# Kernel tuning notes

Measured on AMD Instinct MI355X. Metric: run time of the kernel, lower is better.

The kernel has to match this reference:

```python
import jax, jax.numpy as jnp
import numpy as np

HEADS = 16

def setup_inputs() -> dict:
    key = jax.random.key(0)
    ks = jax.random.split(key, 7)
    B, S, E = 2, 2048, 1024
    return {
        "query": jax.random.normal(ks[0], (B, S, E), dtype=jnp.float32),
        "key": jax.random.normal(ks[1], (B, S, E), dtype=jnp.float32),
        "value": jax.random.normal(ks[2], (B, S, E), dtype=jnp.float32),
        "Wqkv": jax.random.normal(ks[3], (E, 3 * E), dtype=jnp.float32) * (E ** -0.5),
        "bqkv": jax.random.normal(ks[4], (3 * E,), dtype=jnp.float32) * 0.02,
        "Wproj": jax.random.normal(ks[5], (E, E), dtype=jnp.float32) * (E ** -0.5),
        "bproj": jax.random.normal(ks[6], (E,), dtype=jnp.float32) * 0.02,
    }

def reference(query, key, value, Wqkv, bqkv, Wproj, bproj):
    # key/value args are unused in the original forward (overwritten by QKV split)
    B, S, E = query.shape
    H = HEADS
    hd = E // H
    qkv = query @ Wqkv + bqkv                     # [B, S, 3E]
    qkv = qkv.reshape(B, S, H, 3 * hd).transpose(0, 2, 1, 3)  # [B, H, S, 3hd]
    q = qkv[..., :hd]
    k = qkv[..., hd:2 * hd]
    v = qkv[..., 2 * hd:]
    qk = jnp.einsum("bhqd,bhkd->bhqk", q, k)
    # faithful quirk: original divides by head_dim**-0.5, i.e. multiplies by sqrt(hd)
    scaled = qk / (hd ** -0.5)
    attn = jax.nn.softmax(scaled, axis=-1)        # dropout p=0 -> identity
    out = jnp.einsum("bhqk,bhkd->bhqd", attn, v)  # [B, H, S, hd]
    out = out.transpose(0, 2, 1, 3).reshape(B, S, E)
    return out @ Wproj + bproj
```

## Files before the change

### kernel.cpp

```cpp
#include <hip/hip_runtime.h>
#include <hip/hip_bf16.h>
#include <stdint.h>

typedef __attribute__((ext_vector_type(8))) _Float16 f16x8;
typedef __attribute__((ext_vector_type(4))) _Float16 f16x4;
typedef __attribute__((ext_vector_type(4))) float f32x4;

static constexpr int BATCH = 2;
static constexpr int SEQ = 2048;
static constexpr int EMB = 1024;
static constexpr int NH = 16;
static constexpr int HD_ = 64;

#define AS1 __attribute__((address_space(1)))
#define AS3 __attribute__((address_space(3)))

__device__ __forceinline__ void gload_lds16(const void* g, void* l) {
  __builtin_amdgcn_global_load_lds((const AS1 uint32_t*)g, (AS3 uint32_t*)l, 16, 0, 0);
}

__device__ __forceinline__ f32x4 mfma16(f16x8 a, f16x8 b, f32x4 c) {
  return __builtin_amdgcn_mfma_f32_16x16x32_f16(a, b, c, 0, 0, 0);
}

__device__ __forceinline__ f16x8 swzread(const _Float16* base, int row, int blk) {
  return *(const f16x8*)((const char*)base + row * 128 +
                         ((blk * 16) ^ ((row & 7) << 4)));
}

__global__ __launch_bounds__(256) void k_convert(const float* __restrict__ in,
                                                 _Float16* __restrict__ oh, int n4) {
  int idx = blockIdx.x * 256 + threadIdx.x;
  if (idx >= n4) return;
  float4 v = reinterpret_cast<const float4*>(in)[idx];
  const float* f = reinterpret_cast<const float*>(&v);
  _Float16 h[4];
#pragma unroll
  for (int i = 0; i < 4; ++i) h[i] = (_Float16)f[i];
  reinterpret_cast<uint2*>(oh)[idx] = *reinterpret_cast<uint2*>(h);
}

template <int PERM>
__global__ __launch_bounds__(256) void k_transpose(const float* __restrict__ in,
                                                   _Float16* __restrict__ out, int R,
                                                   int C) {
  __shared__ float tile[32][33];
  const int t = threadIdx.x;
  const int tr = t >> 5, tc = t & 31;
  const int r0 = blockIdx.y * 32, c0 = blockIdx.x * 32;
#pragma unroll
  for (int rr = 0; rr < 32; rr += 8)
    tile[tr + rr][tc] = in[(size_t)(r0 + tr + rr) * C + c0 + tc];
  __syncthreads();
#pragma unroll
  for (int rr = 0; rr < 32; rr += 8) {
    const int c = c0 + tr + rr;
    int d = c;
    if constexpr (PERM) {
      const int h = c / 192, r = c - h * 192;
      d = (r < 64) ? h * 64 + r
                   : (r < 128 ? 1024 + h * 64 + (r - 64) : 2048 + h * 64 + (r - 128));
    }
    out[(size_t)d * R + r0 + tc] = (_Float16)tile[tc][tr + rr];
  }
}

__global__ __launch_bounds__(256) void k_gemm_qkv(const _Float16* __restrict__ A,
                                                  const _Float16* __restrict__ Bt,
                                                  const float* __restrict__ bias,
                                                  _Float16* __restrict__ oq,
                                                  _Float16* __restrict__ ok,
                                                  _Float16* __restrict__ ov) {
  constexpr int K = EMB;
  __shared__ _Float16 As[2][128 * 32];
  __shared__ _Float16 Bs[2][128 * 32];
  const int t = threadIdx.x;
  const int l = t & 63, w = t >> 6;
  const int lr = l & 15, lg = l >> 4;
  const int wr = w >> 1, wc = w & 1;
  const int m0 = blockIdx.y * 128, n0 = blockIdx.x * 128;

  auto stage = [&](int buf, int k0) {
#pragma unroll
    for (int j = 0; j < 2; ++j) {
      const int c = t + 256 * j;
      const int row = c >> 2, cb = c & 3;
      gload_lds16(A + (size_t)(m0 + row) * K + k0 + cb * 8, &As[buf][c * 8]);
      gload_lds16(Bt + (size_t)(n0 + row) * K + k0 + cb * 8, &Bs[buf][c * 8]);
    }
  };

  f32x4 acc[4][4];
#pragma unroll
  for (int m = 0; m < 4; ++m)
#pragma unroll
    for (int n = 0; n < 4; ++n) acc[m][n] = f32x4{0.f, 0.f, 0.f, 0.f};

  stage(0, 0);
  const int NT = K / 32;
  int cur = 0;
  for (int kt = 0; kt < NT; ++kt) {
    __syncthreads();
    if (kt + 1 < NT) stage(cur ^ 1, (kt + 1) * 32);
    f16x8 af[4], bf[4];
#pragma unroll
    for (int m = 0; m < 4; ++m)
      af[m] = *(const f16x8*)&As[cur][(wr * 64 + m * 16 + lr) * 32 + lg * 8];
#pragma unroll
    for (int n = 0; n < 4; ++n)
      bf[n] = *(const f16x8*)&Bs[cur][(wc * 64 + n * 16 + lr) * 32 + lg * 8];
#pragma unroll
    for (int m = 0; m < 4; ++m)
#pragma unroll
      for (int n = 0; n < 4; ++n) acc[m][n] = mfma16(af[m], bf[n], acc[m][n]);
    cur ^= 1;
  }

  const int sec = n0 >> 10;
#pragma unroll
  for (int m = 0; m < 4; ++m) {
#pragma unroll
    for (int n = 0; n < 4; ++n) {
      const int col = n0 + wc * 64 + n * 16 + lr;
      const int cc = col & 1023;
      const int h = cc >> 6, r = cc & 63;
      const float bv = bias[h * 192 + sec * 64 + r];
      const int row0 = m0 + wr * 64 + m * 16 + lg * 4;
      const int b = row0 >> 11, s0 = row0 & (SEQ - 1);
      if (sec == 2) {
        f16x4 vv;
#pragma unroll
        for (int i = 0; i < 4; ++i) vv[i] = (_Float16)(acc[m][n][i] + bv);
        *(f16x4*)&ov[(((size_t)b * NH + h) * HD_ + r) * SEQ + s0] = vv;
      } else {
#pragma unroll
        for (int i = 0; i < 4; ++i) {
          const float v = acc[m][n][i] + bv;
          const size_t dst = (((size_t)b * NH + h) * SEQ + s0 + i) * HD_ + r;
          if (sec == 0)
            oq[dst] = (_Float16)(v * 11.5415603f);
          else
            ok[dst] = (_Float16)v;
        }
      }
    }
  }
}

__global__ __launch_bounds__(256) void k_gemm_proj(const _Float16* __restrict__ A,
                                                   const _Float16* __restrict__ Bt,
                                                   const float* __restrict__ bias,
                                                   float* __restrict__ of) {
  constexpr int K = EMB, N = EMB;
  __shared__ _Float16 As[2][128 * 32];
  __shared__ _Float16 Bs[2][128 * 32];
  const int t = threadIdx.x;
  const int l = t & 63, w = t >> 6;
  const int lr = l & 15, lg = l >> 4;
  const int wr = w >> 1, wc = w & 1;
  const int m0 = blockIdx.y * 128, n0 = blockIdx.x * 128;

  auto stage = [&](int buf, int k0) {
#pragma unroll
    for (int j = 0; j < 2; ++j) {
      const int c = t + 256 * j;
      const int row = c >> 2, cb = c & 3;
      gload_lds16(A + (size_t)(m0 + row) * K + k0 + cb * 8, &As[buf][c * 8]);
      gload_lds16(Bt + (size_t)(n0 + row) * K + k0 + cb * 8, &Bs[buf][c * 8]);
    }
  };

  f32x4 acc[4][4];
#pragma unroll
  for (int m = 0; m < 4; ++m)
#pragma unroll
    for (int n = 0; n < 4; ++n) acc[m][n] = f32x4{0.f, 0.f, 0.f, 0.f};

  stage(0, 0);
  const int NT = K / 32;
  int cur = 0;
  for (int kt = 0; kt < NT; ++kt) {
    __syncthreads();
    if (kt + 1 < NT) stage(cur ^ 1, (kt + 1) * 32);
    f16x8 af[4], bf[4];
#pragma unroll
    for (int m = 0; m < 4; ++m)
      af[m] = *(const f16x8*)&As[cur][(wr * 64 + m * 16 + lr) * 32 + lg * 8];
#pragma unroll
    for (int n = 0; n < 4; ++n)
      bf[n] = *(const f16x8*)&Bs[cur][(wc * 64 + n * 16 + lr) * 32 + lg * 8];
#pragma unroll
    for (int m = 0; m < 4; ++m)
#pragma unroll
      for (int n = 0; n < 4; ++n) acc[m][n] = mfma16(af[m], bf[n], acc[m][n]);
    cur ^= 1;
  }

#pragma unroll
  for (int m = 0; m < 4; ++m)
#pragma unroll
    for (int n = 0; n < 4; ++n)
#pragma unroll
      for (int i = 0; i < 4; ++i) {
        const int row = m0 + wr * 64 + m * 16 + lg * 4 + i;
        const int col = n0 + wc * 64 + n * 16 + lr;
        of[(size_t)row * N + col] = acc[m][n][i] + bias[col];
      }
}

__global__ __launch_bounds__(512) void k_attn(
    const _Float16* __restrict__ qs, const _Float16* __restrict__ ks,
    const _Float16* __restrict__ vt, _Float16* __restrict__ op,
    float* __restrict__ marr, float* __restrict__ larr) {
  __shared__ _Float16 Kt[2][64][64];
  __shared__ _Float16 Vt[2][64][64];
  __shared__ _Float16 Pl[8][16][64];
  const int t = threadIdx.x;
  const int l = t & 63, w = t >> 6;
  const int lr = l & 15, lg = l >> 4;
  const int id = blockIdx.x;
  const int xc = id & 7, m_ = id >> 3;
  const int kvh = m_ & 1;
  const int bh = xc + 8 * (m_ >> 5);
  const int qb = ((m_ >> 1) & 15) * 128 + w * 16;
  const int kvbase = kvh * (SEQ / 2);

  const size_t qoff = ((size_t)bh * SEQ + qb + lr) * HD_;
  const f16x8 qf0 = *(const f16x8*)(qs + qoff + lg * 8);
  const f16x8 qf1 = *(const f16x8*)(qs + qoff + 32 + lg * 8);

  const _Float16* kbase = ks + (size_t)bh * SEQ * HD_;
  const _Float16* vbase = vt + (size_t)bh * HD_ * SEQ;

  const int srow = t >> 3, scb = t & 7;
  auto stage = [&](const int buf, const int kv0) {
    gload_lds16(kbase + (size_t)(kv0 + srow) * HD_ + (scb ^ (srow & 7)) * 8,
                &Kt[buf][srow][scb * 8]);
    gload_lds16(vbase + (size_t)srow * SEQ + kv0 + (scb ^ (srow & 7)) * 8,
                &Vt[buf][srow][scb * 8]);
  };

  stage(0, kvbase);

  float mr = -1e30f, lsum = 0.f;
  f32x4 oacc[4];
#pragma unroll
  for (int n = 0; n < 4; ++n) oacc[n] = f32x4{0.f, 0.f, 0.f, 0.f};

  const int NT = SEQ / 128;
  for (int it = 0; it < NT; ++it) {
    const int cur = it & 1;
    __syncthreads();
    if (it + 1 < NT) stage(cur ^ 1, kvbase + (it + 1) * 64);

    f32x4 sa[4];
    __builtin_amdgcn_s_setprio(1);
#pragma unroll
    for (int t4 = 0; t4 < 4; ++t4) {
      const int r = t4 * 16 + lr;
      const f16x8 kf0 = swzread(&Kt[cur][0][0], r, lg);
      const f16x8 kf1 = swzread(&Kt[cur][0][0], r, lg + 4);
      f32x4 s = mfma16(kf0, qf0, f32x4{0.f, 0.f, 0.f, 0.f});
      sa[t4] = mfma16(kf1, qf1, s);
    }
    __builtin_amdgcn_s_setprio(0);

    float t01 = fmaxf(fmaxf(sa[0][0], sa[0][1]), fmaxf(sa[0][2], sa[0][3]));
    float t23 = fmaxf(fmaxf(sa[1][0], sa[1][1]), fmaxf(sa[1][2], sa[1][3]));
    float t45 = fmaxf(fmaxf(sa[2][0], sa[2][1]), fmaxf(sa[2][2], sa[2][3]));
    float t67 = fmaxf(fmaxf(sa[3][0], sa[3][1]), fmaxf(sa[3][2], sa[3][3]));
    float tm = fmaxf(fmaxf(t01, t23), fmaxf(t45, t67));
    tm = fmaxf(tm, __shfl_xor(tm, 16));
    tm = fmaxf(tm, __shfl_xor(tm, 32));

    if (__all(tm < mr - 24.0f)) continue;

    if (__any(tm > mr + 8.0f)) {
      const float nm = fmaxf(mr, tm);
      const float corr = exp2f(mr - nm);
      mr = nm;
      lsum *= corr;
      float cb4[4];
#pragma unroll
      for (int i = 0; i < 4; ++i)
        cb4[i] = __shfl(corr, (l & 48) + ((l >> 4) << 2) + i);
#pragma unroll
      for (int n = 0; n < 4; ++n)
#pragma unroll
        for (int i = 0; i < 4; ++i) oacc[n][i] *= cb4[i];
    }

    float ts = 0.f;
    char* plbase = (char*)&Pl[w][0][0];
#pragma unroll
    for (int t4 = 0; t4 < 4; ++t4) {
      f16x4 pp;
#pragma unroll
      for (int i = 0; i < 4; ++i) {
        const float p = exp2f(sa[t4][i] - mr);
        ts += p;
        pp[i] = (_Float16)p;
      }
      *(f16x4*)(plbase + lr * 128 + ((t4 * 32 + lg * 8) ^ ((lr & 7) << 4))) = pp;
    }
    ts += __shfl_xor(ts, 16);
    ts += __shfl_xor(ts, 32);
    lsum += ts;

    const f16x8 aP0 = swzread(&Pl[w][0][0], lr, lg);
    const f16x8 aP1 = swzread(&Pl[w][0][0], lr, lg + 4);
    __builtin_amdgcn_s_setprio(1);
#pragma unroll
    for (int n = 0; n < 4; ++n) {
      const int d = n * 16 + lr;
      const f16x8 bv0 = swzread(&Vt[cur][0][0], d, lg);
      const f16x8 bv1 = swzread(&Vt[cur][0][0], d, lg + 4);
      oacc[n] = mfma16(aP0, bv0, oacc[n]);
      oacc[n] = mfma16(aP1, bv1, oacc[n]);
    }
    __builtin_amdgcn_s_setprio(0);
  }

  const size_t mlbase = ((size_t)kvh * 32 + bh) * SEQ + qb;
  if (l < 16) {
    marr[mlbase + l] = mr;
    larr[mlbase + l] = lsum;
  }
  _Float16* opb = op + (size_t)kvh * BATCH * SEQ * EMB;
  const int b = bh >> 4, h = bh & 15;
#pragma unroll
  for (int n = 0; n < 4; ++n)
#pragma unroll
    for (int i = 0; i < 4; ++i) {
      const int row = qb + ((l >> 4) << 2) + i;
      opb[((size_t)b * SEQ + row) * EMB + h * HD_ + n * 16 + lr] =
          (_Float16)oacc[n][i];
    }
}

__global__ __launch_bounds__(256) void k_combine(const _Float16* __restrict__ op,
                                                 const float* __restrict__ marr,
                                                 const float* __restrict__ larr,
                                                 _Float16* __restrict__ ao) {
  const int idx = blockIdx.x * 256 + threadIdx.x;
  const int e8 = idx & 127;
  const size_t rs = (size_t)(idx >> 7);
  const int h = e8 >> 3;
  const int b = (int)(rs >> 11);
  const size_t s = rs & (SEQ - 1);
  const size_t mi = ((size_t)b * NH + h) * SEQ + s;
  const float m1 = marr[mi], l1 = larr[mi];
  const float m2 = marr[(size_t)32 * SEQ + mi], l2 = larr[(size_t)32 * SEQ + mi];
  const float mx = fmaxf(m1, m2);
  const float w1 = exp2f(m1 - mx), w2 = exp2f(m2 - mx);
  const float inv = 1.0f / (l1 * w1 + l2 * w2);
  const f16x8 o1 = ((const f16x8*)op)[idx];
  const f16x8 o2 = ((const f16x8*)op)[idx + (BATCH * SEQ * EMB / 8)];
  f16x8 r;
#pragma unroll
  for (int j = 0; j < 8; ++j)
    r[j] = (_Float16)(((float)o1[j] * w1 + (float)o2[j] * w2) * inv);
  ((f16x8*)ao)[idx] = r;
}

extern "C" void kernel_launch(void* const* d_in, const int* in_sizes, int n_in,
                              void* d_out, int out_size, void* d_ws, size_t ws_size,
                              hipStream_t stream) {
  const float* query = (const float*)d_in[0];
  const float* Wqkv = (const float*)d_in[3];
  const float* bqkv = (const float*)d_in[4];
  const float* Wproj = (const float*)d_in[5];
  const float* bproj = (const float*)d_in[6];
  float* out = (float*)d_out;

  char* ws = (char*)d_ws;
  const size_t MB = 1024 * 1024;
  _Float16* q_f16   = (_Float16*)(ws + 0);
  _Float16* Wqkv_t  = (_Float16*)(ws + 16 * MB);
  _Float16* q_s     = (_Float16*)(ws + 24 * MB);
  _Float16* k_s     = (_Float16*)(ws + 32 * MB);
  _Float16* v_t     = (_Float16*)(ws + 40 * MB);
  _Float16* op      = (_Float16*)(ws + 0);
  _Float16* Wproj_t = (_Float16*)(ws + 48 * MB);
  float*    marr    = (float*)(ws + 50 * MB);
  float*    larr    = (float*)(ws + 50 * MB + 512 * 1024);
  _Float16* a_o     = (_Float16*)(ws + 51 * MB);

  const int M = BATCH * SEQ;
  k_convert<<<(M * EMB / 4 + 255) / 256, 256, 0, stream>>>(query, q_f16, M * EMB / 4);
  k_transpose<1><<<dim3(3 * EMB / 32, EMB / 32), 256, 0, stream>>>(Wqkv, Wqkv_t, EMB,
                                                                   3 * EMB);
  k_gemm_qkv<<<dim3(24, M / 128), 256, 0, stream>>>(q_f16, Wqkv_t, bqkv, q_s, k_s, v_t);
  k_transpose<0><<<dim3(EMB / 32, EMB / 32), 256, 0, stream>>>(Wproj, Wproj_t, EMB, EMB);
  k_attn<<<dim3(1024), 512, 0, stream>>>(q_s, k_s, v_t, op, marr, larr);
  k_combine<<<dim3(BATCH * SEQ * EMB / 8 / 256), 256, 0, stream>>>(op, marr, larr, a_o);
  k_gemm_proj<<<dim3(EMB / 128, M / 128), 256, 0, stream>>>(a_o, Wproj_t, bproj, out);
}
```

Baseline: 156.4 us.

## Fuse prep kernels into one launch and split P·V into two halves

Merges the fp16 conversion of the query and both weight transposes into one kernel indexed by block id, which removes two kernel launches and their gaps. In the attention kernel, the P tile is now written and consumed in two 32-column halves through a smaller per-warp LDS buffer with a new swizzle, interleaving the exp computation with the P·V MFMAs. This cuts shared memory use and may allow overlap between the exp work and the matrix ops. The cost is a branchy prep kernel with a runtime perm flag and extra LDS round trips per iteration.

```diff
diff --git a/kernel.cpp b/kernel.cpp
--- a/kernel.cpp
+++ b/kernel.cpp
@@ -28,26 +28,42 @@
                          ((blk * 16) ^ ((row & 7) << 4)));
 }
 
-__global__ __launch_bounds__(256) void k_convert(const float* __restrict__ in,
-                                                 _Float16* __restrict__ oh, int n4) {
-  int idx = blockIdx.x * 256 + threadIdx.x;
-  if (idx >= n4) return;
-  float4 v = reinterpret_cast<const float4*>(in)[idx];
-  const float* f = reinterpret_cast<const float*>(&v);
-  _Float16 h[4];
-#pragma unroll
-  for (int i = 0; i < 4; ++i) h[i] = (_Float16)f[i];
-  reinterpret_cast<uint2*>(oh)[idx] = *reinterpret_cast<uint2*>(h);
-}
-
-template <int PERM>
-__global__ __launch_bounds__(256) void k_transpose(const float* __restrict__ in,
-                                                   _Float16* __restrict__ out, int R,
-                                                   int C) {
+__global__ __launch_bounds__(256) void k_prep(const float* __restrict__ q,
+                                              _Float16* __restrict__ qo,
+                                              const float* __restrict__ wqkv,
+                                              _Float16* __restrict__ wqkvo,
+                                              const float* __restrict__ wproj,
+                                              _Float16* __restrict__ wprojo) {
   __shared__ float tile[32][33];
+  const int blk = blockIdx.x;
   const int t = threadIdx.x;
+  if (blk < 4096) {
+    const int idx = blk * 256 + t;
+    float4 v = reinterpret_cast<const float4*>(q)[idx];
+    const float* f = reinterpret_cast<const float*>(&v);
+    _Float16 h[4];
+#pragma unroll
+    for (int i = 0; i < 4; ++i) h[i] = (_Float16)f[i];
+    reinterpret_cast<uint2*>(qo)[idx] = *reinterpret_cast<uint2*>(h);
+    return;
+  }
+  const float* in;
+  _Float16* out;
+  int R, C, bx, by;
+  bool perm;
+  if (blk < 4096 + 3072) {
+    const int lo = blk - 4096;
+    bx = lo % 96;
+    by = lo / 96;
+    in = wqkv; out = wqkvo; R = 1024; C = 3072; perm = true;
+  } else {
+    const int lo = blk - 7168;
+    bx = lo & 31;
+    by = lo >> 5;
+    in = wproj; out = wprojo; R = 1024; C = 1024; perm = false;
+  }
   const int tr = t >> 5, tc = t & 31;
-  const int r0 = blockIdx.y * 32, c0 = blockIdx.x * 32;
+  const int r0 = by * 32, c0 = bx * 32;
 #pragma unroll
   for (int rr = 0; rr < 32; rr += 8)
     tile[tr + rr][tc] = in[(size_t)(r0 + tr + rr) * C + c0 + tc];
@@ -56,7 +72,7 @@
   for (int rr = 0; rr < 32; rr += 8) {
     const int c = c0 + tr + rr;
     int d = c;
-    if constexpr (PERM) {
+    if (perm) {
       const int h = c / 192, r = c - h * 192;
       d = (r < 64) ? h * 64 + r
                    : (r < 128 ? 1024 + h * 64 + (r - 64) : 2048 + h * 64 + (r - 128));
@@ -214,7 +230,7 @@
     float* __restrict__ marr, float* __restrict__ larr) {
   __shared__ _Float16 Kt[2][64][64];
   __shared__ _Float16 Vt[2][64][64];
-  __shared__ _Float16 Pl[8][16][64];
+  __shared__ _Float16 Plh[8][16][32];
   const int t = threadIdx.x;
   const int l = t & 63, w = t >> 6;
   const int lr = l & 15, lg = l >> 4;
@@ -247,6 +263,9 @@
 #pragma unroll
   for (int n = 0; n < 4; ++n) oacc[n] = f32x4{0.f, 0.f, 0.f, 0.f};
 
+  char* plbase = (char*)&Plh[w][0][0];
+  const int plswz = ((lr >> 1) & 3) << 4;
+
   const int NT = SEQ / 128;
   for (int it = 0; it < NT; ++it) {
     const int cur = it & 1;
@@ -291,34 +310,33 @@
     }
 
     float ts = 0.f;
-    char* plbase = (char*)&Pl[w][0][0];
-#pragma unroll
-    for (int t4 = 0; t4 < 4; ++t4) {
-      f16x4 pp;
-#pragma unroll
-      for (int i = 0; i < 4; ++i) {
-        const float p = exp2f(sa[t4][i] - mr);
-        ts += p;
-        pp[i] = (_Float16)p;
+#pragma unroll
+    for (int H = 0; H < 2; ++H) {
+#pragma unroll
+      for (int th = 0; th < 2; ++th) {
+        const int t4 = 2 * H + th;
+        f16x4 pp;
+#pragma unroll
+        for (int i = 0; i < 4; ++i) {
+          const float p = exp2f(sa[t4][i] - mr);
+          ts += p;
+          pp[i] = (_Float16)p;
+        }
+        *(f16x4*)(plbase + lr * 64 + ((th * 32 + lg * 8) ^ plswz)) = pp;
       }
-      *(f16x4*)(plbase + lr * 128 + ((t4 * 32 + lg * 8) ^ ((lr & 7) << 4))) = pp;
+      const f16x8 aP = *(const f16x8*)(plbase + lr * 64 + ((lg * 16) ^ plswz));
+      __builtin_amdgcn_s_setprio(1);
+#pragma unroll
+      for (int n = 0; n < 4; ++n) {
+        const int d = n * 16 + lr;
+        const f16x8 bv = swzread(&Vt[cur][0][0], d, lg + 4 * H);
+        oacc[n] = mfma16(aP, bv, oacc[n]);
+      }
+      __builtin_amdgcn_s_setprio(0);
     }
     ts += __shfl_xor(ts, 16);
     ts += __shfl_xor(ts, 32);
     lsum += ts;
-
-    const f16x8 aP0 = swzread(&Pl[w][0][0], lr, lg);
-    const f16x8 aP1 = swzread(&Pl[w][0][0], lr, lg + 4);
-    __builtin_amdgcn_s_setprio(1);
-#pragma unroll
-    for (int n = 0; n < 4; ++n) {
-      const int d = n * 16 + lr;
-      const f16x8 bv0 = swzread(&Vt[cur][0][0], d, lg);
-      const f16x8 bv1 = swzread(&Vt[cur][0][0], d, lg + 4);
-      oacc[n] = mfma16(aP0, bv0, oacc[n]);
-      oacc[n] = mfma16(aP1, bv1, oacc[n]);
-    }
-    __builtin_amdgcn_s_setprio(0);
   }
 
   const size_t mlbase = ((size_t)kvh * 32 + bh) * SEQ + qb;
@@ -387,11 +405,8 @@
   _Float16* a_o     = (_Float16*)(ws + 51 * MB);
 
   const int M = BATCH * SEQ;
-  k_convert<<<(M * EMB / 4 + 255) / 256, 256, 0, stream>>>(query, q_f16, M * EMB / 4);
-  k_transpose<1><<<dim3(3 * EMB / 32, EMB / 32), 256, 0, stream>>>(Wqkv, Wqkv_t, EMB,
-                                                                   3 * EMB);
+  k_prep<<<dim3(8192), 256, 0, stream>>>(query, q_f16, Wqkv, Wqkv_t, Wproj, Wproj_t);
   k_gemm_qkv<<<dim3(24, M / 128), 256, 0, stream>>>(q_f16, Wqkv_t, bqkv, q_s, k_s, v_t);
-  k_transpose<0><<<dim3(EMB / 32, EMB / 32), 256, 0, stream>>>(Wproj, Wproj_t, EMB, EMB);
   k_attn<<<dim3(1024), 512, 0, stream>>>(q_s, k_s, v_t, op, marr, larr);
   k_combine<<<dim3(BATCH * SEQ * EMB / 8 / 256), 256, 0, stream>>>(op, marr, larr, a_o);
   k_gemm_proj<<<dim3(EMB / 128, M / 128), 256, 0, stream>>>(a_o, Wproj_t, bproj, out);
```

Measured after the change: 154.1 us. About the same (-1.5%).
